# Kernel tuning notes

Hardware: AMD Instinct MI355X
Metric: run time of the kernel (lower is better)

## Reference

```python
import jax, jax.numpy as jnp
import numpy as np

B, N, T, D = 16, 64, 128, 8
N_EMB, N_H = 64, 128
EPS = 1e-20


def _fully_connected_rel():
    # off-diagonal (receiver, sender) pairs of a fully connected graph
    off = np.ones((N, N)) - np.eye(N)
    rec_idx, send_idx = np.where(off)
    rel_rec = np.eye(N, dtype=np.float32)[rec_idx]
    rel_send = np.eye(N, dtype=np.float32)[send_idx]
    return jnp.asarray(rel_rec), jnp.asarray(rel_send)


def setup_inputs() -> dict:
    key = jax.random.key(0)
    ks = jax.random.split(key, 8)
    inputs = jax.random.normal(ks[0], (B, N, T, D), dtype=jnp.float32)
    rel_rec, rel_send = _fully_connected_rel()
    s = 0.05
    Wc = jax.random.normal(ks[1], (N_EMB, D), dtype=jnp.float32) * s
    bc = jnp.zeros((N_EMB,), jnp.float32)
    Ws = jax.random.normal(ks[2], (N_EMB, D), dtype=jnp.float32) * s
    bs = jnp.zeros((N_EMB,), jnp.float32)
    F_in = 2 * N_EMB
    W_ih = jax.random.normal(ks[3], (4 * N_H, F_in), dtype=jnp.float32) * s
    W_hh = jax.random.normal(ks[4], (4 * N_H, N_H), dtype=jnp.float32) * s
    b_ih = jnp.zeros((4 * N_H,), jnp.float32)
    b_hh = jnp.zeros((4 * N_H,), jnp.float32)
    return {"inputs": inputs, "rel_rec": rel_rec, "rel_send": rel_send,
            "Wc": Wc, "bc": bc, "Ws": Ws, "bs": bs,
            "W_ih": W_ih, "W_hh": W_hh, "b_ih": b_ih, "b_hh": b_hh}


def _gcn(x, rel_rec, rel_send, Wc, bc, Ws, bs):
    # x: [B, N, T, D]; rel_*: [E, N] one-hot
    senders = jnp.einsum('en,bntd->betd', rel_send, x)      # [B,E,T,D]
    receivers = jnp.einsum('en,bntd->betd', rel_rec, x)
    diff = receivers - senders
    spatial_norm = jnp.sqrt(jnp.sum(diff * diff, axis=-1))  # [B,E,T]
    vals = 1.0 / (spatial_norm + EPS)
    vals = jnp.transpose(vals, (0, 2, 1))                   # [B,T,E]
    # A = rel_send^T diag(vals) rel_rec, without the ExE diag_embed
    A = jnp.einsum('es,bte,er->btsr', rel_send, vals, rel_rec)  # [B,T,N,N]
    rowsum = jnp.sum(A, axis=-1, keepdims=True)
    A = A / jnp.clip(rowsum, 1e-12)                         # row-normalized
    x_t = jnp.transpose(x, (0, 2, 1, 3))                    # [B,T,N,D]
    x_conv = jnp.einsum('btnm,btmd->btnd', A, x_t) @ Wc.T + bc  # [B,T,N,emb]
    x_conv = jnp.transpose(x_conv, (0, 2, 1, 3))            # [B,N,T,emb]
    x_skip = x @ Ws.T + bs                                  # [B,N,T,emb]
    return jax.nn.selu(jnp.concatenate([x_skip, x_conv], axis=-1))


def _lstm(x_seq, W_ih, W_hh, b_ih, b_hh):
    # x_seq: [T, BN, F]
    BN = x_seq.shape[1]
    h0 = jnp.zeros((BN, N_H), x_seq.dtype)
    c0 = jnp.zeros((BN, N_H), x_seq.dtype)

    def step(carry, x_t):
        h, c = carry
        gates = x_t @ W_ih.T + b_ih + h @ W_hh.T + b_hh
        i, f, g, o = jnp.split(gates, 4, axis=-1)
        c = jax.nn.sigmoid(f) * c + jax.nn.sigmoid(i) * jnp.tanh(g)
        h = jax.nn.sigmoid(o) * jnp.tanh(c)
        return (h, c), None

    (h, c), _ = jax.lax.scan(step, (h0, c0), x_seq)
    return h


def reference(inputs, rel_rec, rel_send, Wc, bc, Ws, bs, W_ih, W_hh, b_ih, b_hh):
    b, n, t, _ = inputs.shape
    x = _gcn(inputs, rel_rec, rel_send, Wc, bc, Ws, bs)     # [B,N,T,2*emb]
    x_seq = jnp.transpose(x, (2, 0, 1, 3)).reshape(t, b * n, -1)
    h = _lstm(x_seq, W_ih, W_hh, b_ih, b_hh)                # [B*N, n_h]
    return h.reshape(b, n, -1)
```

## Files before the change

### kernel.cpp

```cpp
#include <hip/hip_runtime.h>
#include <hip/hip_bf16.h>


typedef _Float16 half8 __attribute__((ext_vector_type(8)));
typedef float f32x4 __attribute__((ext_vector_type(4)));

__device__ __forceinline__ float rcp_(float x){ return __builtin_amdgcn_rcpf(x); }
__device__ __forceinline__ float sigmoidf_(float x){ return rcp_(1.0f + __expf(-x)); }
__device__ __forceinline__ float tanhf_(float x){ return fmaf(-2.0f, rcp_(1.0f + __expf(2.0f*x)), 1.0f); }

__global__ __launch_bounds__(256) void prep_kernel(const float* __restrict__ W_ih,
                                                   const float* __restrict__ W_hh,
                                                   _Float16* __restrict__ wfrag){
  int gid = blockIdx.x*256 + threadIdx.x;
  int w    = gid >> 11;
  int i    = (gid >> 6) & 31;
  int lane = gid & 63;
  int src = i >> 4, kk = (i >> 2) & 3, cti = i & 3;
  int j = 16*w + 128*cti + (lane & 15);
  int kbase = 32*kk + 8*(lane >> 4);
  const float* W = src ? W_hh : W_ih;
  _Float16* dst = wfrag + (size_t)(((w*32 + i)*64 + lane) * 8);
  #pragma unroll
  for (int e = 0; e < 8; e++) dst[e] = (_Float16)W[j*128 + kbase + e];
}

__global__ __launch_bounds__(256) void gcn2_kernel(const float* __restrict__ x,
    const float* __restrict__ Wc, const float* __restrict__ bc,
    const float* __restrict__ Ws, const float* __restrict__ bs,
    _Float16* __restrict__ feat){
  __shared__ _Float16 W2[32*136];
  __shared__ _Float16 As16[4][64*72];
  __shared__ _Float16 zs16[4][64*40];

  int tid = threadIdx.x;
  int wav = tid >> 6, lane = tid & 63;
  int slice = blockIdx.x*4 + wav;
  int b = slice >> 7, t = slice & 127;
  int c = lane & 15, kq = lane >> 4;

  for (int idx = tid; idx < 32*136; idx += 256){
    int k = idx / 136, f = idx - k*136;
    float v = 0.f;
    if (f < 64){
      if (k < 8) v = Ws[f*8 + k];
      else if (k == 16) v = bs[f];
    } else if (f < 128){
      if (k >= 8 && k < 16) v = Wc[(f-64)*8 + (k-8)];
      else if (k == 16) v = bc[f-64];
    }
    W2[idx] = (_Float16)v;
  }

  _Float16* As_w = &As16[wav][0];
  _Float16* zs_w = &zs16[wav][0];

  const float* xrow = x + ((size_t)(b*64 + lane)*128 + t)*8;
  float4 xlo = *(const float4*)xrow;
  float4 xhi = *(const float4*)(xrow + 4);
  float xr[8] = {xlo.x, xlo.y, xlo.z, xlo.w, xhi.x, xhi.y, xhi.z, xhi.w};
  {
    half8 hx;
    #pragma unroll
    for (int d = 0; d < 8; d++) hx[d] = (_Float16)xr[d];
    half8 h1 = (half8){(_Float16)1.f,0,0,0,0,0,0,0};
    half8 h0 = (half8){0,0,0,0,0,0,0,0};
    *(half8*)(zs_w + lane*40)      = hx;
    *(half8*)(zs_w + lane*40 + 8)  = h1;
    *(half8*)(zs_w + lane*40 + 16) = h1;
    *(half8*)(zs_w + lane*40 + 24) = h0;
  }

  #pragma unroll 4
  for (int m = 0; m < 64; m++){
    float d2 = 0.f;
    #pragma unroll
    for (int d = 0; d < 8; d++){
      float xm = __int_as_float(__builtin_amdgcn_readlane(__float_as_int(xr[d]), m));
      float df = xm - xr[d];
      d2 = fmaf(df, df, d2);
    }
    float wv = (m == lane) ? 0.f : __frsqrt_rn(d2);
    As_w[m*72 + lane] = (_Float16)wv;
  }

  __syncthreads();

  half8 wfr[8];
  #pragma unroll
  for (int nt = 0; nt < 8; nt++){
    half8 tmp;
    #pragma unroll
    for (int e = 0; e < 8; e++) tmp[e] = W2[(8*kq + e)*136 + 16*nt + c];
    wfr[nt] = tmp;
  }

  half8 bx0, bx1;
  {
    half8 t0, t1;
    #pragma unroll
    for (int e = 0; e < 8; e++){
      t0[e] = zs_w[(8*kq + e)*40 + c];
      t1[e] = zs_w[(32 + 8*kq + e)*40 + c];
    }
    bx0 = t0; bx1 = t1;
  }

  const f32x4 zero4 = (f32x4){0.f,0.f,0.f,0.f};

  #pragma unroll
  for (int mt = 0; mt < 4; mt++){
    half8 aa0 = *(const half8*)(As_w + (16*mt + c)*72 + 8*kq);
    half8 aa1 = *(const half8*)(As_w + (16*mt + c)*72 + 32 + 8*kq);
    f32x4 cax = __builtin_amdgcn_mfma_f32_16x16x32_f16(aa0, bx0, zero4, 0,0,0);
    cax = __builtin_amdgcn_mfma_f32_16x16x32_f16(aa1, bx1, cax, 0,0,0);
    int bidx = ((lane & 48) | 8) << 2;
    #pragma unroll
    for (int e = 0; e < 4; e++){
      float rs = __int_as_float(__builtin_amdgcn_ds_bpermute(bidx, __float_as_int(cax[e])));
      float yv = cax[e] * rcp_(fmaxf(rs, 1e-12f));
      if (c < 8) zs_w[(16*mt + 4*kq + e)*40 + 8 + c] = (_Float16)yv;
    }
  }

  #pragma unroll
  for (int mt = 0; mt < 4; mt++){
    half8 az = *(const half8*)(zs_w + (16*mt + c)*40 + 8*kq);
    #pragma unroll
    for (int nt = 0; nt < 8; nt++){
      f32x4 pc = __builtin_amdgcn_mfma_f32_16x16x32_f16(az, wfr[nt], zero4, 0,0,0);
      #pragma unroll
      for (int e = 0; e < 4; e++){
        float v = pc[e];
        v = (v > 0.f) ? 1.0507009873554805f*v
                      : 1.7580993408473766f*(__expf(v) - 1.0f);
        feat[((size_t)t*1024 + (size_t)b*64 + 16*mt + 4*kq + e)*128 + 16*nt + c] = (_Float16)v;
      }
    }
  }
}

__global__ __launch_bounds__(512, 2) void lstm3_kernel(
    const _Float16* __restrict__ wfrag, const _Float16* __restrict__ feat,
    const float* __restrict__ b_ih, const float* __restrict__ b_hh,
    float* __restrict__ out){
  int tid = threadIdx.x;
  int w = tid >> 6, l = tid & 63;
  int blk = blockIdx.x;
  int r = l & 15, kq = l >> 4;
  __shared__ _Float16 h_lds[2][544];

  half8 bf[32];
  const _Float16* wb = wfrag + (size_t)w*(32*64*8);
  #pragma unroll
  for (int i = 0; i < 32; i++)
    bf[i] = *(const half8*)(wb + (size_t)(i*64 + l)*8);

  f32x4 biasx4[4];
  #pragma unroll
  for (int cti = 0; cti < 4; cti++){
    int j = 16*w + 128*cti + r;
    float bv = b_ih[j] + b_hh[j];
    biasx4[cti] = (f32x4){bv, bv, bv, bv};
  }

  for (int idx = tid; idx < 544; idx += 512) h_lds[0][idx] = (_Float16)0.f;

  float cc = 0.f, hlast = 0.f;
  const f32x4 zero4 = (f32x4){0.f,0.f,0.f,0.f};

  const size_t arow_s = (size_t)(blk*4 + (r >> 2));
  const int atl = r & 3;
  const int habase = (r & 3)*134 + 8*kq;

  half8 afA[4], afB[4];
  f32x4 accxA[4], accxB[4];

#define LOADAF(AF, G) {                                                       \
    int gg = (G) > 31 ? 31 : (G);                                             \
    const _Float16* fb = feat + ((size_t)(4*gg + atl)*1024 + arow_s)*128 + 8*kq; \
    AF[0] = *(const half8*)(fb);                                              \
    AF[1] = *(const half8*)(fb + 32);                                         \
    AF[2] = *(const half8*)(fb + 64);                                         \
    AF[3] = *(const half8*)(fb + 96);                                         \
  }

  LOADAF(afA, 0)
  #pragma unroll
  for (int cti = 0; cti < 4; cti++)
    accxA[cti] = __builtin_amdgcn_mfma_f32_16x16x32_f16(afA[0], bf[cti], biasx4[cti], 0,0,0);
  #pragma unroll
  for (int kk = 1; kk < 4; kk++)
    #pragma unroll
    for (int cti = 0; cti < 4; cti++)
      accxA[cti] = __builtin_amdgcn_mfma_f32_16x16x32_f16(afA[kk], bf[kk*4+cti], accxA[cti], 0,0,0);
  LOADAF(afB, 1)
  LOADAF(afA, 2)
  __syncthreads();

#define SEL(A) ((kq & 2) ? ((kq & 1) ? A[3] : A[2]) : ((kq & 1) ? A[1] : A[0]))

#define STEP3(TL, ACCU, ACCB, AFB_, GN)                                       \
  {                                                                           \
    half8 ha[4];                                                              \
    _Pragma("unroll")                                                         \
    for (int kk = 0; kk < 4; kk++)                                            \
      ha[kk] = *(const half8*)(&h_lds[(TL)&1][habase + 32*kk]);               \
    f32x4 acc0, acc1, acc2, acc3;                                             \
    acc0 = __builtin_amdgcn_mfma_f32_16x16x32_f16(ha[0], bf[16], zero4, 0,0,0); \
    acc1 = __builtin_amdgcn_mfma_f32_16x16x32_f16(ha[0], bf[17], zero4, 0,0,0); \
    acc2 = __builtin_amdgcn_mfma_f32_16x16x32_f16(ha[0], bf[18], zero4, 0,0,0); \
    acc3 = __builtin_amdgcn_mfma_f32_16x16x32_f16(ha[0], bf[19], zero4, 0,0,0); \
    _Pragma("unroll")                                                         \
    for (int kk = 1; kk < 4; kk++){                                           \
      acc0 = __builtin_amdgcn_mfma_f32_16x16x32_f16(ha[kk], bf[16+kk*4+0], acc0, 0,0,0); \
      acc1 = __builtin_amdgcn_mfma_f32_16x16x32_f16(ha[kk], bf[16+kk*4+1], acc1, 0,0,0); \
      acc2 = __builtin_amdgcn_mfma_f32_16x16x32_f16(ha[kk], bf[16+kk*4+2], acc2, 0,0,0); \
      acc3 = __builtin_amdgcn_mfma_f32_16x16x32_f16(ha[kk], bf[16+kk*4+3], acc3, 0,0,0); \
    }                                                                         \
    _Pragma("unroll")                                                         \
    for (int cti = 0; cti < 4; cti++){                                        \
      if ((TL) == 0)                                                          \
        ACCB[cti] = __builtin_amdgcn_mfma_f32_16x16x32_f16(AFB_[0], bf[cti], biasx4[cti], 0,0,0); \
      else                                                                    \
        ACCB[cti] = __builtin_amdgcn_mfma_f32_16x16x32_f16(AFB_[(TL)], bf[(TL)*4+cti], ACCB[cti], 0,0,0); \
    }                                                                         \
    if ((TL) == 3) LOADAF(AFB_, GN)                                           \
    float g0_ = SEL(acc0) + ACCU[0][(TL)];                                    \
    float g1_ = SEL(acc1) + ACCU[1][(TL)];                                    \
    float g2_ = SEL(acc2) + ACCU[2][(TL)];                                    \
    float g3_ = SEL(acc3) + ACCU[3][(TL)];                                    \
    float c_ = fmaf(sigmoidf_(g1_), cc, sigmoidf_(g0_)*tanhf_(g2_));          \
    cc = c_;                                                                  \
    float h_ = sigmoidf_(g3_)*tanhf_(c_);                                     \
    h_lds[1-((TL)&1)][kq*134 + 16*w + r] = (_Float16)h_;                      \
    hlast = h_;                                                               \
    asm volatile("s_waitcnt lgkmcnt(0)" ::: "memory");                        \
    __builtin_amdgcn_s_barrier();                                             \
  }

  for (int i = 0; i < 16; ++i){
    STEP3(0, accxA, accxB, afB, 0)
    STEP3(1, accxA, accxB, afB, 0)
    STEP3(2, accxA, accxB, afB, 0)
    STEP3(3, accxA, accxB, afB, 2*i+3)
    STEP3(0, accxB, accxA, afA, 0)
    STEP3(1, accxB, accxA, afA, 0)
    STEP3(2, accxB, accxA, afA, 0)
    STEP3(3, accxB, accxA, afA, 2*i+4)
  }
#undef STEP3
#undef SEL
#undef LOADAF

  out[((size_t)blk*4 + kq)*128 + 16*w + r] = hlast;
}

extern "C" void kernel_launch(void* const* d_in, const int* in_sizes, int n_in,
                              void* d_out, int out_size, void* d_ws, size_t ws_size,
                              hipStream_t stream) {
  const float* x    = (const float*)d_in[0];
  const float* Wc   = (const float*)d_in[3];
  const float* bc   = (const float*)d_in[4];
  const float* Ws   = (const float*)d_in[5];
  const float* bs   = (const float*)d_in[6];
  const float* W_ih = (const float*)d_in[7];
  const float* W_hh = (const float*)d_in[8];
  const float* b_ih = (const float*)d_in[9];
  const float* b_hh = (const float*)d_in[10];
  float* out = (float*)d_out;

  _Float16* wfrag = (_Float16*)d_ws;
  _Float16* feat  = (_Float16*)((char*)d_ws + 262144);

  prep_kernel<<<64, 256, 0, stream>>>(W_ih, W_hh, wfrag);
  gcn2_kernel<<<512, 256, 0, stream>>>(x, Wc, bc, Ws, bs, feat);
  lstm3_kernel<<<256, 512, 0, stream>>>(wfrag, feat, b_ih, b_hh, out);
}
```

Before: 116.8 us.

## Compute pairwise distances via MFMA Gram matrix and prebuild GCN weight fragments

Replaces the per-lane readlane loop for pairwise squared distances with a Gram-matrix MFMA, using |a|^2+|b|^2-2ab. The rowsum column now comes from a constant ones operand. The GCN weight fragments are built once in prep_kernel instead of in every block through LDS, and the LSTM loop peels its last iteration so hlast is written only once. The fp16 Gram formulation can lose precision for close points, which matters because rsqrt amplifies small distances.

```diff
diff --git a/kernel.cpp b/kernel.cpp
--- a/kernel.cpp
+++ b/kernel.cpp
@@ -11,8 +11,32 @@
 
 __global__ __launch_bounds__(256) void prep_kernel(const float* __restrict__ W_ih,
                                                    const float* __restrict__ W_hh,
-                                                   _Float16* __restrict__ wfrag){
+                                                   const float* __restrict__ Wc,
+                                                   const float* __restrict__ bc,
+                                                   const float* __restrict__ Ws,
+                                                   const float* __restrict__ bs,
+                                                   _Float16* __restrict__ wfrag,
+                                                   _Float16* __restrict__ w2frag){
   int gid = blockIdx.x*256 + threadIdx.x;
+  if (gid < 512){
+    int nt = gid >> 6, lane = gid & 63;
+    int kq = lane >> 4, c = lane & 15;
+    _Float16* dst2 = w2frag + (size_t)(nt*64 + lane)*8;
+    #pragma unroll
+    for (int e = 0; e < 8; e++){
+      int k = 8*kq + e;
+      int f = 16*nt + c;
+      float v = 0.f;
+      if (f < 64){
+        if (k < 8) v = Ws[f*8 + k];
+        else if (k == 16) v = bs[f];
+      } else {
+        if (k >= 8 && k < 16) v = Wc[(f-64)*8 + (k-8)];
+        else if (k == 16) v = bc[f-64];
+      }
+      dst2[e] = (_Float16)v;
+    }
+  }
   int w    = gid >> 11;
   int i    = (gid >> 6) & 31;
   int lane = gid & 63;
@@ -25,13 +49,11 @@
   for (int e = 0; e < 8; e++) dst[e] = (_Float16)W[j*128 + kbase + e];
 }
 
-__global__ __launch_bounds__(256) void gcn2_kernel(const float* __restrict__ x,
-    const float* __restrict__ Wc, const float* __restrict__ bc,
-    const float* __restrict__ Ws, const float* __restrict__ bs,
-    _Float16* __restrict__ feat){
-  __shared__ _Float16 W2[32*136];
+__global__ __launch_bounds__(256) void gcn3_kernel(const float* __restrict__ x,
+    const _Float16* __restrict__ w2frag, _Float16* __restrict__ feat){
   __shared__ _Float16 As16[4][64*72];
   __shared__ _Float16 zs16[4][64*40];
+  __shared__ float    ns16[4][64];
 
   int tid = threadIdx.x;
   int wav = tid >> 6, lane = tid & 63;
@@ -39,21 +61,9 @@
   int b = slice >> 7, t = slice & 127;
   int c = lane & 15, kq = lane >> 4;
 
-  for (int idx = tid; idx < 32*136; idx += 256){
-    int k = idx / 136, f = idx - k*136;
-    float v = 0.f;
-    if (f < 64){
-      if (k < 8) v = Ws[f*8 + k];
-      else if (k == 16) v = bs[f];
-    } else if (f < 128){
-      if (k >= 8 && k < 16) v = Wc[(f-64)*8 + (k-8)];
-      else if (k == 16) v = bc[f-64];
-    }
-    W2[idx] = (_Float16)v;
-  }
-
   _Float16* As_w = &As16[wav][0];
   _Float16* zs_w = &zs16[wav][0];
+  float*    ns_w = &ns16[wav][0];
 
   const float* xrow = x + ((size_t)(b*64 + lane)*128 + t)*8;
   float4 xlo = *(const float4*)xrow;
@@ -61,38 +71,31 @@
   float xr[8] = {xlo.x, xlo.y, xlo.z, xlo.w, xhi.x, xhi.y, xhi.z, xhi.w};
   {
     half8 hx;
-    #pragma unroll
-    for (int d = 0; d < 8; d++) hx[d] = (_Float16)xr[d];
-    half8 h1 = (half8){(_Float16)1.f,0,0,0,0,0,0,0};
+    float nrm = 0.f;
+    #pragma unroll
+    for (int d = 0; d < 8; d++){ hx[d] = (_Float16)xr[d]; nrm = fmaf(xr[d], xr[d], nrm); }
     half8 h0 = (half8){0,0,0,0,0,0,0,0};
     *(half8*)(zs_w + lane*40)      = hx;
-    *(half8*)(zs_w + lane*40 + 8)  = h1;
+    *(half8*)(zs_w + lane*40 + 8)  = h0;
+    *(half8*)(zs_w + lane*40 + 16) = h0;
+    *(half8*)(zs_w + lane*40 + 24) = h0;
+    ns_w[lane] = nrm;
+  }
+
+  half8 wfr[8];
+  #pragma unroll
+  for (int nt = 0; nt < 8; nt++)
+    wfr[nt] = *(const half8*)(w2frag + (size_t)(nt*64 + lane)*8);
+
+  half8 ga[4];
+  #pragma unroll
+  for (int q = 0; q < 4; q++)
+    ga[q] = *(const half8*)(zs_w + (16*q + c)*40 + 8*kq);
+
+  asm volatile("s_waitcnt lgkmcnt(0)" ::: "memory");
+  {
+    half8 h1 = (half8){(_Float16)1.f,0,0,0,0,0,0,0};
     *(half8*)(zs_w + lane*40 + 16) = h1;
-    *(half8*)(zs_w + lane*40 + 24) = h0;
-  }
-
-  #pragma unroll 4
-  for (int m = 0; m < 64; m++){
-    float d2 = 0.f;
-    #pragma unroll
-    for (int d = 0; d < 8; d++){
-      float xm = __int_as_float(__builtin_amdgcn_readlane(__float_as_int(xr[d]), m));
-      float df = xm - xr[d];
-      d2 = fmaf(df, df, d2);
-    }
-    float wv = (m == lane) ? 0.f : __frsqrt_rn(d2);
-    As_w[m*72 + lane] = (_Float16)wv;
-  }
-
-  __syncthreads();
-
-  half8 wfr[8];
-  #pragma unroll
-  for (int nt = 0; nt < 8; nt++){
-    half8 tmp;
-    #pragma unroll
-    for (int e = 0; e < 8; e++) tmp[e] = W2[(8*kq + e)*136 + 16*nt + c];
-    wfr[nt] = tmp;
   }
 
   half8 bx0, bx1;
@@ -103,10 +106,37 @@
       t0[e] = zs_w[(8*kq + e)*40 + c];
       t1[e] = zs_w[(32 + 8*kq + e)*40 + c];
     }
-    bx0 = t0; bx1 = t1;
+    half8 h1a = (half8){(_Float16)1.f,(_Float16)1.f,(_Float16)1.f,(_Float16)1.f,
+                        (_Float16)1.f,(_Float16)1.f,(_Float16)1.f,(_Float16)1.f};
+    bx0 = (c == 8) ? h1a : t0;
+    bx1 = (c == 8) ? h1a : t1;
+  }
+
+  f32x4 nm[4];
+  float nn[4];
+  #pragma unroll
+  for (int q = 0; q < 4; q++){
+    nm[q] = *(const f32x4*)(ns_w + 16*q + 4*kq);
+    nn[q] = ns_w[16*q + c];
   }
 
   const f32x4 zero4 = (f32x4){0.f,0.f,0.f,0.f};
+  int ediag = c - 4*kq;
+
+  #pragma unroll
+  for (int mt = 0; mt < 4; mt++){
+    #pragma unroll
+    for (int nt = 0; nt < 4; nt++){
+      f32x4 g = __builtin_amdgcn_mfma_f32_16x16x32_f16(ga[mt], ga[nt], zero4, 0,0,0);
+      #pragma unroll
+      for (int e = 0; e < 4; e++){
+        float d2 = nm[mt][e] + nn[nt] - 2.0f*g[e];
+        float wv = __frsqrt_rn(fmaxf(d2, 1e-12f));
+        if (mt == nt && e == ediag) wv = 0.f;
+        As_w[(16*mt + 4*kq + e)*72 + 16*nt + c] = (_Float16)wv;
+      }
+    }
+  }
 
   #pragma unroll
   for (int mt = 0; mt < 4; mt++){
@@ -234,12 +264,12 @@
     cc = c_;                                                                  \
     float h_ = sigmoidf_(g3_)*tanhf_(c_);                                     \
     h_lds[1-((TL)&1)][kq*134 + 16*w + r] = (_Float16)h_;                      \
-    hlast = h_;                                                               \
+    if ((TL) == 3 && (GN) == 32) hlast = h_;                                  \
     asm volatile("s_waitcnt lgkmcnt(0)" ::: "memory");                        \
     __builtin_amdgcn_s_barrier();                                             \
   }
 
-  for (int i = 0; i < 16; ++i){
+  for (int i = 0; i < 15; ++i){
     STEP3(0, accxA, accxB, afB, 0)
     STEP3(1, accxA, accxB, afB, 0)
     STEP3(2, accxA, accxB, afB, 0)
@@ -249,6 +279,14 @@
     STEP3(2, accxB, accxA, afA, 0)
     STEP3(3, accxB, accxA, afA, 2*i+4)
   }
+  STEP3(0, accxA, accxB, afB, 0)
+  STEP3(1, accxA, accxB, afB, 0)
+  STEP3(2, accxA, accxB, afB, 0)
+  STEP3(3, accxA, accxB, afB, 33)
+  STEP3(0, accxB, accxA, afA, 0)
+  STEP3(1, accxB, accxA, afA, 0)
+  STEP3(2, accxB, accxA, afA, 0)
+  STEP3(3, accxB, accxA, afA, 32)
 #undef STEP3
 #undef SEL
 #undef LOADAF
@@ -270,10 +308,11 @@
   const float* b_hh = (const float*)d_in[10];
   float* out = (float*)d_out;
 
-  _Float16* wfrag = (_Float16*)d_ws;
-  _Float16* feat  = (_Float16*)((char*)d_ws + 262144);
-
-  prep_kernel<<<64, 256, 0, stream>>>(W_ih, W_hh, wfrag);
-  gcn2_kernel<<<512, 256, 0, stream>>>(x, Wc, bc, Ws, bs, feat);
+  _Float16* wfrag  = (_Float16*)d_ws;
+  _Float16* w2frag = (_Float16*)((char*)d_ws + 262144);
+  _Float16* feat   = (_Float16*)((char*)d_ws + 270336);
+
+  prep_kernel<<<64, 256, 0, stream>>>(W_ih, W_hh, Wc, bc, Ws, bs, wfrag, w2frag);
+  gcn3_kernel<<<512, 256, 0, stream>>>(x, w2frag, feat);
   lstm3_kernel<<<256, 512, 0, stream>>>(wfrag, feat, b_ih, b_hh, out);
 }
```

Result: faster. 103.5 us (median of 3 runs) (-11.4%).
